# Optimization experiments

Hardware: AMD Instinct MI355X
Metric: run time of the kernel (lower is better)

## Reference

```python
import jax, jax.numpy as jnp
import numpy as np

NUM_HEADS = 16
GRID_SIZE = 16


def rotate(x, pos):
    # x: [B, nH, N, D] with D even; pos: [N] float
    D = x.shape[-1]
    half = D // 2
    omega = jnp.arange(half, dtype=x.dtype) / half
    omega = 1.0 / (10000.0 ** omega)
    freq = pos[:, None].astype(x.dtype) * omega          # [N, half]
    # torch .repeat(1,1,1,2) TILES the last dim (not interleave)
    emb_sin = jnp.tile(jnp.sin(freq), (1, 2))            # [N, D]
    emb_cos = jnp.tile(jnp.cos(freq), (1, 2))
    y = x.reshape(x.shape[:-1] + (half, 2))
    rot = jnp.stack((-y[..., 1], y[..., 0]), axis=-1).reshape(x.shape)
    return x * emb_cos + rot * emb_sin


def setup_inputs() -> dict:
    key = jax.random.key(0)
    k1, k2, k3, k4 = jax.random.split(key, 4)
    B, N, C = 2, 2048, 1024
    return {
        "x": jax.random.normal(k1, (B, N, C), dtype=jnp.float32),
        "W_qkv": jax.random.normal(k2, (3 * C, C), dtype=jnp.float32) * 0.02,
        "W_proj": jax.random.normal(k3, (C, C), dtype=jnp.float32) * 0.02,
        "b_proj": jax.random.normal(k4, (C,), dtype=jnp.float32) * 0.02,
        "T": 8,
        "H": 16,
        "W": 16,
    }


def reference(x, W_qkv, W_proj, b_proj, T, H, W):
    B, N, C = x.shape
    nH = NUM_HEADS
    hd = C // nH
    d_dim = 2 * (hd // 3 // 2)   # 20 for hd=64
    h_dim = d_dim
    w_dim = d_dim

    # axial positions (mask=None path): ids = arange(T*H*W)
    ids = jnp.arange(T * H * W)
    d_pos = (ids // (H * W)).astype(jnp.float32)
    rem = ids % (H * W)
    h_pos = (rem // W).astype(jnp.float32) * (GRID_SIZE / H)
    w_pos = (rem % W).astype(jnp.float32) * (GRID_SIZE / W)

    # fused QKV projection (no bias)
    qkv = jnp.einsum('bnc,oc->bno', x, W_qkv)            # [B, N, 3C]
    qkv = qkv.reshape(B, N, 3, nH, hd).transpose(2, 0, 3, 1, 4)
    q, k, v = qkv[0], qkv[1], qkv[2]                     # [B, nH, N, hd]

    s0, s1, s2 = 0, d_dim, d_dim + h_dim
    s3 = s2 + w_dim
    qd = rotate(q[..., s0:s1], d_pos); kd = rotate(k[..., s0:s1], d_pos)
    qh = rotate(q[..., s1:s2], h_pos); kh = rotate(k[..., s1:s2], h_pos)
    qw = rotate(q[..., s2:s3], w_pos); kw = rotate(k[..., s2:s3], w_pos)
    if s3 < hd:
        q = jnp.concatenate([qd, qh, qw, q[..., s3:]], axis=-1)
        k = jnp.concatenate([kd, kh, kw, k[..., s3:]], axis=-1)
    else:
        q = jnp.concatenate([qd, qh, qw], axis=-1)
        k = jnp.concatenate([kd, kh, kw], axis=-1)

    # SDPA (default scale = hd**-0.5, no dropout, not causal)
    scale = hd ** (-0.5)
    scores = jnp.einsum('bhqd,bhkd->bhqk', q, k) * scale
    attn = jax.nn.softmax(scores, axis=-1)
    out = jnp.einsum('bhqk,bhkd->bhqd', attn, v)          # [B, nH, N, hd]

    out = out.transpose(0, 2, 1, 3).reshape(B, N, C)
    out = jnp.einsum('bnc,oc->bno', out, W_proj) + b_proj
    return out


if __name__ == "__main__":
    inp = setup_inputs()
    y = reference(**inp)
    print(y.shape, y.dtype)
```

## Files before the change

### kernel.cpp

```cpp
#include <hip/hip_runtime.h>
#include <stdint.h>

typedef unsigned short u16;
typedef __attribute__((ext_vector_type(8))) short bf16x8;
typedef __attribute__((ext_vector_type(4))) float f32x4;

#define DEVI static __device__ __forceinline__

static constexpr int NTOK = 2048;
static constexpr int CDIM = 1024;
static constexpr int C3   = 3072;

DEVI u16 f2bf(float f) {
  uint32_t u = __float_as_uint(f);
  return (u16)((u + 0x7fffu + ((u >> 16) & 1u)) >> 16);
}

DEVI float exp2fast(float x) { return __builtin_amdgcn_exp2f(x); }

DEVI void gl_lds16(const void* g, void* l) {
  __builtin_amdgcn_global_load_lds(
      (__attribute__((address_space(1))) uint32_t*)g,
      (__attribute__((address_space(3))) uint32_t*)l, 16, 0, 0);
}

DEVI f32x4 mfma16(bf16x8 a, bf16x8 b, f32x4 c) {
  return __builtin_amdgcn_mfma_f32_16x16x32_bf16(a, b, c, 0, 0, 0);
}

__global__ void k_cvt(const float* __restrict__ in, u16* __restrict__ out, int n) {
  int i = (blockIdx.x * blockDim.x + threadIdx.x) * 4;
  if (i >= n) return;
  float4 v = *reinterpret_cast<const float4*>(in + i);
  ushort4 o;
  o.x = f2bf(v.x); o.y = f2bf(v.y); o.z = f2bf(v.z); o.w = f2bf(v.w);
  *reinterpret_cast<ushort4*>(out + i) = o;
}

template<int MODE>
__global__ __launch_bounds__(256, 2) void k_gemm(
    const u16* __restrict__ A, const u16* __restrict__ Bw,
    float* __restrict__ Cout, const float* __restrict__ bias,
    u16* __restrict__ qb, u16* __restrict__ kb, u16* __restrict__ vb,
    int Nn, int K) {
  __shared__ u16 Al[128 * 32];
  __shared__ u16 Bl[128 * 32];
  const int tid = threadIdx.x, wid = tid >> 6, lane = tid & 63;
  const int bm = blockIdx.x, bn = blockIdx.y;
  const int wr = wid >> 1, wc = wid & 1;
  f32x4 acc[4][4] = {};

  const int r0 = wid * 16 + (lane >> 2);
  const int c0 = (lane & 3) * 8;
  const u16* Ag = A + (size_t)(bm * 128) * K + c0;
  const u16* Bg = Bw + (size_t)(bn * 128) * K + c0;
  u16* Alb = Al + wid * 512;
  u16* Blb = Bl + wid * 512;
  const int fr = lane & 15, fk = (lane >> 4) * 8;

  for (int kt = 0; kt < K; kt += 32) {
    __syncthreads();
    gl_lds16(Ag + (size_t)r0 * K + kt,        Alb);
    gl_lds16(Ag + (size_t)(64 + r0) * K + kt, Alb + 2048);
    gl_lds16(Bg + (size_t)r0 * K + kt,        Blb);
    gl_lds16(Bg + (size_t)(64 + r0) * K + kt, Blb + 2048);
    __syncthreads();
    bf16x8 af[4], bfr[4];
#pragma unroll
    for (int i = 0; i < 4; ++i)
      af[i] = *reinterpret_cast<const bf16x8*>(&Al[(wr * 64 + i * 16 + fr) * 32 + fk]);
#pragma unroll
    for (int j = 0; j < 4; ++j)
      bfr[j] = *reinterpret_cast<const bf16x8*>(&Bl[(wc * 64 + j * 16 + fr) * 32 + fk]);
#pragma unroll
    for (int i = 0; i < 4; ++i)
#pragma unroll
      for (int j = 0; j < 4; ++j)
        acc[i][j] = mfma16(af[i], bfr[j], acc[i][j]);
  }
  const int orow0 = bm * 128 + wr * 64 + (lane >> 4) * 4;

  if constexpr (MODE == 1) {
    const int ocol0 = bn * 128 + wc * 64 + fr;
#pragma unroll
    for (int j = 0; j < 4; ++j) {
      int col = ocol0 + j * 16;
      float badd = bias[col];
#pragma unroll
      for (int i = 0; i < 4; ++i)
#pragma unroll
        for (int r = 0; r < 4; ++r)
          Cout[(size_t)(orow0 + i * 16 + r) * Nn + col] = acc[i][j][r] + badd;
    }
  } else {
    const int which = bn >> 3;
    const int cbase = (bn & 7) * 128 + wc * 64 + fr;
    u16* dst = (which == 0) ? qb : (which == 1) ? kb : vb;
#pragma unroll
    for (int j = 0; j < 4; ++j) {
      const int c = cbase + j * 16;
      const int d = c & 63, hh = c >> 6;
      const bool dorope = (which != 2) && (d < 60);
      int seg = 0; float omega = 0.f;
      if (dorope) {
        seg = d / 20;
        int ds = d - seg * 20;
        int jj = (ds >= 10) ? ds - 10 : ds;
        omega = exp2fast(-1.3287712379549449f * (float)jj);
      }
#pragma unroll
      for (int i = 0; i < 4; ++i) {
#pragma unroll
        for (int r = 0; r < 4; ++r) {
          const int m = orow0 + i * 16 + r;
          const int b = m >> 11, n = m & (NTOK - 1);
          float val = acc[i][j][r];
          float pr = __shfl_xor(val, 1, 64);
          float outv = val;
          if (dorope) {
            float pos = (seg == 0) ? (float)(n >> 8)
                      : (seg == 1) ? (float)((n >> 4) & 15)
                                   : (float)(n & 15);
            float f = pos * omega, sn, cs;
            __sincosf(f, &sn, &cs);
            outv = (d & 1) ? val * cs + pr * sn : val * cs - pr * sn;
          }
          if (which == 0) outv *= 0.18033688011112042f;
          dst[((size_t)(b * 16 + hh) * NTOK + n) * 64 + d] = f2bf(outv);
        }
      }
    }
  }
}

__global__ void k_vt(const u16* __restrict__ vb, u16* __restrict__ vT) {
  __shared__ u16 tile[64][72];
  const int bh = blockIdx.x;
  const int n0 = blockIdx.y * 64;
  const int t = threadIdx.x;
  const int nr = t >> 2, cq = (t & 3) * 16;
  const u16* src = vb + ((size_t)bh * NTOK + n0 + nr) * 64 + cq;
  *reinterpret_cast<bf16x8*>(&tile[nr][cq])     = *reinterpret_cast<const bf16x8*>(src);
  *reinterpret_cast<bf16x8*>(&tile[nr][cq + 8]) = *reinterpret_cast<const bf16x8*>(src + 8);
  __syncthreads();
  const int d = t >> 2, nq = (t & 3) * 16;
  u16 buf[16];
#pragma unroll
  for (int i = 0; i < 16; ++i) buf[i] = tile[nq + i][d];
  u16* dst = vT + ((size_t)bh * 64 + d) * NTOK + n0 + nq;
  *reinterpret_cast<bf16x8*>(dst)     = *reinterpret_cast<const bf16x8*>(&buf[0]);
  *reinterpret_cast<bf16x8*>(dst + 8) = *reinterpret_cast<const bf16x8*>(&buf[8]);
}

__global__ __launch_bounds__(256, 2) void k_attn(
    const u16* __restrict__ qb, const u16* __restrict__ kb,
    const u16* __restrict__ vT, u16* __restrict__ outb) {
  __shared__ u16 Kl[2][64 * 64];
  __shared__ u16 Vl[2][64 * 64];
  __shared__ u16 Pl[4][32 * 64];
  const int bh = blockIdx.x;
  const int qt = blockIdx.y;
  const int tid = threadIdx.x, wid = tid >> 6, lane = tid & 63;
  const int fr = lane & 15, fg = lane >> 4;
  const int swz = fr & 7;

  bf16x8 qf[2][2];
  const u16* qbase = qb + ((size_t)bh * NTOK + qt * 128 + wid * 32 + fr) * 64;
#pragma unroll
  for (int qa = 0; qa < 2; ++qa)
#pragma unroll
    for (int h = 0; h < 2; ++h)
      qf[qa][h] = *reinterpret_cast<const bf16x8*>(qbase + qa * 1024 + h * 32 + fg * 8);

  f32x4 acc[2][4] = {};
  float mrun[2] = {-1e30f, -1e30f}, lrun[2] = {0.f, 0.f};

  const int srow = lane >> 3;
  const int scol = ((lane & 7) ^ srow) * 8;
  const u16* kg = kb + ((size_t)bh * NTOK + wid * 8 + srow) * 64 + scol;
  const u16* vg = vT + ((size_t)bh * 64 + wid * 8 + srow) * NTOK + scol;
  u16* Pw = &Pl[wid][0];

  auto stage = [&](int buf, int kvt) {
#pragma unroll
    for (int s = 0; s < 2; ++s) {
      gl_lds16(kg + (size_t)(kvt + s * 32) * 64, &Kl[buf][s * 2048 + wid * 512]);
      gl_lds16(vg + (size_t)(s * 32) * NTOK + kvt, &Vl[buf][s * 2048 + wid * 512]);
    }
  };

  stage(0, 0);
  __syncthreads();
  int cur = 0;
  for (int kvt = 0; kvt < NTOK; kvt += 64) {
    if (kvt + 64 < NTOK) stage(cur ^ 1, kvt + 64);
    const u16* Kc = &Kl[cur][0];
    const u16* Vc = &Vl[cur][0];

    bf16x8 kf[4][2], vf[4][2];
#pragma unroll
    for (int mf = 0; mf < 4; ++mf) {
      int rb = (mf * 16 + fr) * 64;
#pragma unroll
      for (int h = 0; h < 2; ++h)
        kf[mf][h] = *reinterpret_cast<const bf16x8*>(Kc + rb + (((h * 4 + fg) ^ swz) * 8));
    }
#pragma unroll
    for (int nf = 0; nf < 4; ++nf) {
      int rb = (nf * 16 + fr) * 64;
#pragma unroll
      for (int ks = 0; ks < 2; ++ks)
        vf[nf][ks] = *reinterpret_cast<const bf16x8*>(Vc + rb + (((ks * 4 + fg) ^ swz) * 8));
    }

    f32x4 st[2][4];
    __builtin_amdgcn_s_setprio(1);
#pragma unroll
    for (int qa = 0; qa < 2; ++qa)
#pragma unroll
      for (int mf = 0; mf < 4; ++mf) {
        f32x4 s0 = {};
        s0 = mfma16(kf[mf][0], qf[qa][0], s0);
        s0 = mfma16(kf[mf][1], qf[qa][1], s0);
        st[qa][mf] = s0;
      }
    __builtin_amdgcn_s_setprio(0);

    float corrA[2]; bool skipA[2];
#pragma unroll
    for (int qa = 0; qa < 2; ++qa) {
      float t0 = fmaxf(fmaxf(st[qa][0][0], st[qa][0][1]), fmaxf(st[qa][0][2], st[qa][0][3]));
      float t1 = fmaxf(fmaxf(st[qa][1][0], st[qa][1][1]), fmaxf(st[qa][1][2], st[qa][1][3]));
      float t2 = fmaxf(fmaxf(st[qa][2][0], st[qa][2][1]), fmaxf(st[qa][2][2], st[qa][2][3]));
      float t3 = fmaxf(fmaxf(st[qa][3][0], st[qa][3][1]), fmaxf(st[qa][3][2], st[qa][3][3]));
      float tm = fmaxf(fmaxf(t0, t1), fmaxf(t2, t3));
      tm = fmaxf(tm, __shfl_xor(tm, 16, 64));
      tm = fmaxf(tm, __shfl_xor(tm, 32, 64));
      skipA[qa] = (__all(tm - mrun[qa] <= 8.f) != 0);
      float mref;
      if (skipA[qa]) {
        corrA[qa] = 1.f; mref = mrun[qa];
      } else {
        float mnew = fmaxf(mrun[qa], tm);
        corrA[qa] = exp2fast(mrun[qa] - mnew);
        mrun[qa] = mnew; mref = mnew;
      }
      float ps = 0.f;
      const int prow = qa * 16 + fr;
#pragma unroll
      for (int mf = 0; mf < 4; ++mf) {
        float p0 = exp2fast(st[qa][mf][0] - mref);
        float p1 = exp2fast(st[qa][mf][1] - mref);
        float p2 = exp2fast(st[qa][mf][2] - mref);
        float p3 = exp2fast(st[qa][mf][3] - mref);
        ps += (p0 + p1) + (p2 + p3);
        uint32_t k0, k1;
        asm("v_cvt_pk_bf16_f32 %0, %1, %2" : "=v"(k0) : "v"(p0), "v"(p1));
        asm("v_cvt_pk_bf16_f32 %0, %1, %2" : "=v"(k1) : "v"(p2), "v"(p3));
        int c16 = (mf * 2 + (fg >> 1)) ^ swz;
        uint2 val; val.x = k0; val.y = k1;
        *reinterpret_cast<uint2*>(Pw + prow * 64 + c16 * 8 + (fg & 1) * 4) = val;
      }
      ps += __shfl_xor(ps, 16, 64);
      ps += __shfl_xor(ps, 32, 64);
      lrun[qa] = lrun[qa] * corrA[qa] + ps;
    }

    __builtin_amdgcn_sched_barrier(0);
    asm volatile("s_waitcnt lgkmcnt(0)" ::: "memory");
    __builtin_amdgcn_sched_barrier(0);

#pragma unroll
    for (int qa = 0; qa < 2; ++qa) {
      if (!skipA[qa]) {
        float cr[4];
#pragma unroll
        for (int r = 0; r < 4; ++r) cr[r] = __shfl(corrA[qa], fg * 4 + r, 64);
#pragma unroll
        for (int nf = 0; nf < 4; ++nf)
#pragma unroll
          for (int r = 0; r < 4; ++r) acc[qa][nf][r] *= cr[r];
      }
      const int prow = qa * 16 + fr;
      bf16x8 pa[2];
#pragma unroll
      for (int ks = 0; ks < 2; ++ks)
        pa[ks] = *reinterpret_cast<const bf16x8*>(Pw + prow * 64 + (((ks * 4 + fg) ^ swz) * 8));
      __builtin_amdgcn_s_setprio(1);
#pragma unroll
      for (int nf = 0; nf < 4; ++nf)
#pragma unroll
        for (int ks = 0; ks < 2; ++ks)
          acc[qa][nf] = mfma16(pa[ks], vf[nf][ks], acc[qa][nf]);
      __builtin_amdgcn_s_setprio(0);
    }
    __syncthreads();
    cur ^= 1;
  }

  const int b = bh >> 4, h = bh & 15;
#pragma unroll
  for (int qa = 0; qa < 2; ++qa) {
    float linv[4];
#pragma unroll
    for (int r = 0; r < 4; ++r) linv[r] = 1.f / __shfl(lrun[qa], fg * 4 + r, 64);
#pragma unroll
    for (int nf = 0; nf < 4; ++nf)
#pragma unroll
      for (int r = 0; r < 4; ++r) {
        int n = qt * 128 + wid * 32 + qa * 16 + fg * 4 + r;
        int col = h * 64 + nf * 16 + fr;
        outb[((size_t)b * NTOK + n) * CDIM + col] = f2bf(acc[qa][nf][r] * linv[r]);
      }
  }
}

extern "C" void kernel_launch(void* const* d_in, const int* in_sizes, int n_in,
                              void* d_out, int out_size, void* d_ws, size_t ws_size,
                              hipStream_t stream) {
  (void)in_sizes; (void)n_in; (void)out_size; (void)ws_size;
  const float* x  = (const float*)d_in[0];
  const float* Wq = (const float*)d_in[1];
  const float* Wp = (const float*)d_in[2];
  const float* bp = (const float*)d_in[3];

  char* w = (char*)d_ws;
  u16* x_bf  = (u16*)(w + 0);
  u16* wq_bf = (u16*)(w + 8388608);
  u16* wp_bf = (u16*)(w + 14680064);
  u16* q_bf  = (u16*)(w + 16777216);
  u16* k_bf  = (u16*)(w + 25165824);
  u16* v_bf  = (u16*)(w + 33554432);
  u16* vT    = (u16*)(w + 41943040);
  u16* at_bf = (u16*)(w + 50331648);

  k_cvt<<<4096, 256, 0, stream>>>(x,  x_bf,  4194304);
  k_cvt<<<3072, 256, 0, stream>>>(Wq, wq_bf, 3145728);
  k_cvt<<<1024, 256, 0, stream>>>(Wp, wp_bf, 1048576);

  k_gemm<2><<<dim3(32, 24), 256, 0, stream>>>(x_bf, wq_bf, nullptr, nullptr,
                                              q_bf, k_bf, v_bf, C3, CDIM);

  k_vt<<<dim3(32, 32), 256, 0, stream>>>(v_bf, vT);

  k_attn<<<dim3(32, 16), 256, 0, stream>>>(q_bf, k_bf, vT, at_bf);

  k_gemm<1><<<dim3(32, 8), 256, 0, stream>>>(at_bf, wp_bf, (float*)d_out, bp,
                                             nullptr, nullptr, nullptr, CDIM, CDIM);
}
```

Measured before the change: 141.4 us.

## Fuse V transpose into QKV GEMM epilogue and merge conversion kernels

New measurement: 128.3 us. -9.3%, faster.

```diff
diff --git a/kernel.cpp b/kernel.cpp
--- a/kernel.cpp
+++ b/kernel.cpp
@@ -28,26 +28,33 @@
   return __builtin_amdgcn_mfma_f32_16x16x32_bf16(a, b, c, 0, 0, 0);
 }
 
-__global__ void k_cvt(const float* __restrict__ in, u16* __restrict__ out, int n) {
+__global__ void k_cvt3(const float* __restrict__ x, const float* __restrict__ wq,
+                       const float* __restrict__ wp, u16* __restrict__ xb,
+                       u16* __restrict__ wqb, u16* __restrict__ wpb) {
   int i = (blockIdx.x * blockDim.x + threadIdx.x) * 4;
-  if (i >= n) return;
-  float4 v = *reinterpret_cast<const float4*>(in + i);
+  const float* src; u16* dst; int off;
+  if (i < 4194304)      { src = x;  dst = xb;  off = i; }
+  else if (i < 7340032) { src = wq; dst = wqb; off = i - 4194304; }
+  else                  { src = wp; dst = wpb; off = i - 7340032; }
+  float4 v = *reinterpret_cast<const float4*>(src + off);
   ushort4 o;
   o.x = f2bf(v.x); o.y = f2bf(v.y); o.z = f2bf(v.z); o.w = f2bf(v.w);
-  *reinterpret_cast<ushort4*>(out + i) = o;
+  *reinterpret_cast<ushort4*>(dst + off) = o;
 }
 
 template<int MODE>
 __global__ __launch_bounds__(256, 2) void k_gemm(
     const u16* __restrict__ A, const u16* __restrict__ Bw,
     float* __restrict__ Cout, const float* __restrict__ bias,
-    u16* __restrict__ qb, u16* __restrict__ kb, u16* __restrict__ vb,
+    u16* __restrict__ qb, u16* __restrict__ kb, u16* __restrict__ vT,
     int Nn, int K) {
-  __shared__ u16 Al[128 * 32];
-  __shared__ u16 Bl[128 * 32];
+  __shared__ u16 smem[MODE == 2 ? 17408 : 8192];
+  u16* Al = smem;
+  u16* Bl = smem + 4096;
   const int tid = threadIdx.x, wid = tid >> 6, lane = tid & 63;
   const int bm = blockIdx.x, bn = blockIdx.y;
   const int wr = wid >> 1, wc = wid & 1;
+  const int fr = lane & 15, fg = lane >> 4;
   f32x4 acc[4][4] = {};
 
   const int r0 = wid * 16 + (lane >> 2);
@@ -56,7 +63,7 @@
   const u16* Bg = Bw + (size_t)(bn * 128) * K + c0;
   u16* Alb = Al + wid * 512;
   u16* Blb = Bl + wid * 512;
-  const int fr = lane & 15, fk = (lane >> 4) * 8;
+  const int fk = fg * 8;
 
   for (int kt = 0; kt < K; kt += 32) {
     __syncthreads();
@@ -78,7 +85,7 @@
       for (int j = 0; j < 4; ++j)
         acc[i][j] = mfma16(af[i], bfr[j], acc[i][j]);
   }
-  const int orow0 = bm * 128 + wr * 64 + (lane >> 4) * 4;
+  const int orow0 = bm * 128 + wr * 64 + fg * 4;
 
   if constexpr (MODE == 1) {
     const int ocol0 = bn * 128 + wc * 64 + fr;
@@ -94,62 +101,69 @@
     }
   } else {
     const int which = bn >> 3;
-    const int cbase = (bn & 7) * 128 + wc * 64 + fr;
-    u16* dst = (which == 0) ? qb : (which == 1) ? kb : vb;
-#pragma unroll
-    for (int j = 0; j < 4; ++j) {
-      const int c = cbase + j * 16;
-      const int d = c & 63, hh = c >> 6;
-      const bool dorope = (which != 2) && (d < 60);
-      int seg = 0; float omega = 0.f;
-      if (dorope) {
-        seg = d / 20;
-        int ds = d - seg * 20;
-        int jj = (ds >= 10) ? ds - 10 : ds;
-        omega = exp2fast(-1.3287712379549449f * (float)jj);
-      }
-#pragma unroll
-      for (int i = 0; i < 4; ++i) {
-#pragma unroll
-        for (int r = 0; r < 4; ++r) {
-          const int m = orow0 + i * 16 + r;
-          const int b = m >> 11, n = m & (NTOK - 1);
-          float val = acc[i][j][r];
-          float pr = __shfl_xor(val, 1, 64);
-          float outv = val;
-          if (dorope) {
-            float pos = (seg == 0) ? (float)(n >> 8)
-                      : (seg == 1) ? (float)((n >> 4) & 15)
-                                   : (float)(n & 15);
-            float f = pos * omega, sn, cs;
-            __sincosf(f, &sn, &cs);
-            outv = (d & 1) ? val * cs + pr * sn : val * cs - pr * sn;
+    if (which < 2) {
+      const int cbase = (bn & 7) * 128 + wc * 64 + fr;
+      u16* dst = (which == 0) ? qb : kb;
+#pragma unroll
+      for (int j = 0; j < 4; ++j) {
+        const int c = cbase + j * 16;
+        const int d = c & 63, hh = c >> 6;
+        const bool dorope = (d < 60);
+        int seg = 0; float omega = 0.f;
+        if (dorope) {
+          seg = d / 20;
+          int ds = d - seg * 20;
+          int jj = (ds >= 10) ? ds - 10 : ds;
+          omega = exp2fast(-1.3287712379549449f * (float)jj);
+        }
+#pragma unroll
+        for (int i = 0; i < 4; ++i) {
+#pragma unroll
+          for (int r = 0; r < 4; ++r) {
+            const int m = orow0 + i * 16 + r;
+            const int b = m >> 11, n = m & (NTOK - 1);
+            float val = acc[i][j][r];
+            float pr = __shfl_xor(val, 1, 64);
+            float outv = val;
+            if (dorope) {
+              float pos = (seg == 0) ? (float)(n >> 8)
+                        : (seg == 1) ? (float)((n >> 4) & 15)
+                                     : (float)(n & 15);
+              float f = pos * omega, sn, cs;
+              __sincosf(f, &sn, &cs);
+              outv = (d & 1) ? val * cs + pr * sn : val * cs - pr * sn;
+            }
+            if (which == 0) outv *= 0.18033688011112042f;
+            dst[((size_t)(b * 16 + hh) * NTOK + n) * 64 + d] = f2bf(outv);
           }
-          if (which == 0) outv *= 0.18033688011112042f;
-          dst[((size_t)(b * 16 + hh) * NTOK + n) * 64 + d] = f2bf(outv);
         }
       }
+    } else {
+      __syncthreads();
+      const int mbase = wr * 64 + fg * 4;
+#pragma unroll
+      for (int j = 0; j < 4; ++j) {
+        const int crow = wc * 64 + j * 16 + fr;
+#pragma unroll
+        for (int i = 0; i < 4; ++i) {
+          ushort4 pk;
+          pk.x = f2bf(acc[i][j][0]); pk.y = f2bf(acc[i][j][1]);
+          pk.z = f2bf(acc[i][j][2]); pk.w = f2bf(acc[i][j][3]);
+          *reinterpret_cast<ushort4*>(&smem[crow * 136 + mbase + i * 16]) = pk;
+        }
+      }
+      __syncthreads();
+      const int c = tid >> 1, mh = (tid & 1) * 64;
+      const int cfull = (bn & 7) * 128 + c;
+      const int hh = cfull >> 6, d = cfull & 63;
+      const int b = bm >> 4;
+      u16* dst = vT + (((size_t)(b * 16 + hh)) * 64 + d) * NTOK + (bm & 15) * 128 + mh;
+      const u16* srcl = &smem[c * 136 + mh];
+#pragma unroll
+      for (int s = 0; s < 8; ++s)
+        *reinterpret_cast<bf16x8*>(dst + s * 8) = *reinterpret_cast<const bf16x8*>(srcl + s * 8);
     }
   }
-}
-
-__global__ void k_vt(const u16* __restrict__ vb, u16* __restrict__ vT) {
-  __shared__ u16 tile[64][72];
-  const int bh = blockIdx.x;
-  const int n0 = blockIdx.y * 64;
-  const int t = threadIdx.x;
-  const int nr = t >> 2, cq = (t & 3) * 16;
-  const u16* src = vb + ((size_t)bh * NTOK + n0 + nr) * 64 + cq;
-  *reinterpret_cast<bf16x8*>(&tile[nr][cq])     = *reinterpret_cast<const bf16x8*>(src);
-  *reinterpret_cast<bf16x8*>(&tile[nr][cq + 8]) = *reinterpret_cast<const bf16x8*>(src + 8);
-  __syncthreads();
-  const int d = t >> 2, nq = (t & 3) * 16;
-  u16 buf[16];
-#pragma unroll
-  for (int i = 0; i < 16; ++i) buf[i] = tile[nq + i][d];
-  u16* dst = vT + ((size_t)bh * 64 + d) * NTOK + n0 + nq;
-  *reinterpret_cast<bf16x8*>(dst)     = *reinterpret_cast<const bf16x8*>(&buf[0]);
-  *reinterpret_cast<bf16x8*>(dst + 8) = *reinterpret_cast<const bf16x8*>(&buf[8]);
 }
 
 __global__ __launch_bounds__(256, 2) void k_attn(
@@ -226,7 +240,6 @@
       }
     __builtin_amdgcn_s_setprio(0);
 
-    float corrA[2]; bool skipA[2];
 #pragma unroll
     for (int qa = 0; qa < 2; ++qa) {
       float t0 = fmaxf(fmaxf(st[qa][0][0], st[qa][0][1]), fmaxf(st[qa][0][2], st[qa][0][3]));
@@ -236,13 +249,13 @@
       float tm = fmaxf(fmaxf(t0, t1), fmaxf(t2, t3));
       tm = fmaxf(tm, __shfl_xor(tm, 16, 64));
       tm = fmaxf(tm, __shfl_xor(tm, 32, 64));
-      skipA[qa] = (__all(tm - mrun[qa] <= 8.f) != 0);
-      float mref;
-      if (skipA[qa]) {
-        corrA[qa] = 1.f; mref = mrun[qa];
+      bool skip = (__all(tm - mrun[qa] <= 8.f) != 0);
+      float corr, mref;
+      if (skip) {
+        corr = 1.f; mref = mrun[qa];
       } else {
         float mnew = fmaxf(mrun[qa], tm);
-        corrA[qa] = exp2fast(mrun[qa] - mnew);
+        corr = exp2fast(mrun[qa] - mnew);
         mrun[qa] = mnew; mref = mnew;
       }
       float ps = 0.f;
@@ -263,25 +276,19 @@
       }
       ps += __shfl_xor(ps, 16, 64);
       ps += __shfl_xor(ps, 32, 64);
-      lrun[qa] = lrun[qa] * corrA[qa] + ps;
-    }
-
-    __builtin_amdgcn_sched_barrier(0);
-    asm volatile("s_waitcnt lgkmcnt(0)" ::: "memory");
-    __builtin_amdgcn_sched_barrier(0);
-
-#pragma unroll
-    for (int qa = 0; qa < 2; ++qa) {
-      if (!skipA[qa]) {
+      lrun[qa] = lrun[qa] * corr + ps;
+
+      asm volatile("" ::: "memory");
+
+      if (!skip) {
         float cr[4];
 #pragma unroll
-        for (int r = 0; r < 4; ++r) cr[r] = __shfl(corrA[qa], fg * 4 + r, 64);
+        for (int r = 0; r < 4; ++r) cr[r] = __shfl(corr, fg * 4 + r, 64);
 #pragma unroll
         for (int nf = 0; nf < 4; ++nf)
 #pragma unroll
           for (int r = 0; r < 4; ++r) acc[qa][nf][r] *= cr[r];
       }
-      const int prow = qa * 16 + fr;
       bf16x8 pa[2];
 #pragma unroll
       for (int ks = 0; ks < 2; ++ks)
@@ -330,18 +337,13 @@
   u16* wp_bf = (u16*)(w + 14680064);
   u16* q_bf  = (u16*)(w + 16777216);
   u16* k_bf  = (u16*)(w + 25165824);
-  u16* v_bf  = (u16*)(w + 33554432);
-  u16* vT    = (u16*)(w + 41943040);
-  u16* at_bf = (u16*)(w + 50331648);
-
-  k_cvt<<<4096, 256, 0, stream>>>(x,  x_bf,  4194304);
-  k_cvt<<<3072, 256, 0, stream>>>(Wq, wq_bf, 3145728);
-  k_cvt<<<1024, 256, 0, stream>>>(Wp, wp_bf, 1048576);
+  u16* vT    = (u16*)(w + 33554432);
+  u16* at_bf = (u16*)(w + 41943040);
+
+  k_cvt3<<<8192, 256, 0, stream>>>(x, Wq, Wp, x_bf, wq_bf, wp_bf);
 
   k_gemm<2><<<dim3(32, 24), 256, 0, stream>>>(x_bf, wq_bf, nullptr, nullptr,
-                                              q_bf, k_bf, v_bf, C3, CDIM);
-
-  k_vt<<<dim3(32, 32), 256, 0, stream>>>(v_bf, vT);
+                                              q_bf, k_bf, vT, C3, CDIM);
 
   k_attn<<<dim3(32, 16), 256, 0, stream>>>(q_bf, k_bf, vT, at_bf);
 
```
